# Kernel optimization log

Measured on AMD Instinct MI355X. Metric: run time of the kernel, lower is better.

## Reference

```python
import jax, jax.numpy as jnp
import numpy as np

N_NODES = 4096
D_MODEL = 1024
MAX_DEPS = 8
N_CLASSES = 64


def setup_inputs() -> dict:
    key = jax.random.key(0)
    k1, k2, k3 = jax.random.split(key, 3)
    questions = jax.random.normal(k1, (N_NODES, D_MODEL), dtype=jnp.float32)
    # Padded dependency lists; every dependency index is strictly < node index,
    # so processing nodes in index order is a valid topological order.
    rng = np.random.default_rng(0)
    dep_idx = np.zeros((N_NODES, MAX_DEPS), dtype=np.int32)
    dep_mask = np.zeros((N_NODES, MAX_DEPS), dtype=np.int32)
    for i in range(1, N_NODES):
        nd = int(rng.integers(1, MAX_DEPS + 1))
        dep_idx[i, :nd] = rng.integers(0, i, size=nd)
        dep_mask[i, :nd] = 1
    W1 = jax.random.normal(k2, (D_MODEL, 2 * D_MODEL), dtype=jnp.float32) * 0.02
    b1 = jnp.zeros((D_MODEL,), dtype=jnp.float32)
    W2 = jax.random.normal(k3, (N_CLASSES, D_MODEL), dtype=jnp.float32) * 0.02
    b2 = jnp.zeros((N_CLASSES,), dtype=jnp.float32)
    return {
        "questions": questions,
        "W1": W1,
        "b1": b1,
        "W2": W2,
        "b2": b2,
        "dep_idx": jnp.asarray(dep_idx),
        "dep_mask": jnp.asarray(dep_mask),
    }


def reference(questions, W1, b1, W2, b2, dep_idx, dep_mask):
    n_nodes, d_model = questions.shape

    def step(answers, xs):
        i, q, deps, mask = xs
        ctx = answers[deps]                       # [MAX_DEPS, d_model] gather
        m = mask.astype(q.dtype)
        # masked mean; all-zero mask -> zero context (matches torch zeros branch)
        ctx_mean = (ctx * m[:, None]).sum(0) / jnp.maximum(m.sum(), 1.0)
        combined = jnp.concatenate([q, ctx_mean])  # [2*d_model]
        h = jax.nn.gelu(combined @ W1.T + b1, approximate=False)
        return answers.at[i].set(h), None

    answers0 = jnp.zeros((n_nodes, d_model), dtype=questions.dtype)
    xs = (jnp.arange(n_nodes), questions, dep_idx, dep_mask)
    answers, _ = jax.lax.scan(step, answers0, xs)
    root_answer = answers[n_nodes - 1]            # root = last node in topo order
    return root_answer @ W2.T + b2                # [n_classes] logits
```

## Files before the change

### kernel.cpp

```cpp
#include <hip/hip_runtime.h>

#define NN 4096
#define DM 1024
#define MD 8
#define NW 256
#define NCOL 4
#define NT 512
#define NWAVE (NT / 64)
#define UR 4
#define MAXL 4097

#define MI_NLEV 0
#define MI_ROOTPOS 1
#define MI_ARRIVE 8
#define MI_LO 1024
#define MI_NL 6144
#define MI_PERM 10240
#define MI_DCNT 14336
#define MI_INV 18432
#define MI_DPOS 22528

typedef __attribute__((ext_vector_type(8))) short bf16x8;
typedef __attribute__((ext_vector_type(8))) unsigned short ushort8;
typedef __attribute__((ext_vector_type(4))) float f32x4;

__device__ __forceinline__ float gelu_f(float x) {
  return 0.5f * x * (1.0f + erff(x * 0.70710678118654752440f));
}
__device__ __forceinline__ unsigned short f2bf(float x) {
  unsigned int u = __builtin_bit_cast(unsigned int, x);
  u += 0x7FFFu + ((u >> 16) & 1u);
  return (unsigned short)(u >> 16);
}
__device__ __forceinline__ float bf2f(unsigned short v) {
  return __builtin_bit_cast(float, (unsigned int)v << 16);
}

__global__ __launch_bounds__(1024) void k_prologue(
    const int* __restrict__ dep_idx, const int* __restrict__ dep_mask,
    int* __restrict__ meta) {
  __shared__ int lvl[NN];
  __shared__ int cnt[2 * NN];
  __shared__ int pos[NN];
  __shared__ int liv[NN];
  __shared__ int s_changed, s_max;
  const int t = threadIdx.x;
  for (int i = t; i < NN; i += 1024) { lvl[i] = 0; pos[i] = 0; liv[i] = (i == NN - 1) ? 1 : 0; }
  for (int i = t; i < 2 * NN; i += 1024) cnt[i] = 0;
  if (t == 0) s_max = 0;
  __syncthreads();
  for (int u = 0; u < 4; ++u) {
    const int i = u * 1024 + t;
    const int4 d0 = *(const int4*)&dep_idx[i * MD];
    const int4 d1 = *(const int4*)&dep_idx[i * MD + 4];
    const int4 m0 = *(const int4*)&dep_mask[i * MD];
    const int4 m1 = *(const int4*)&dep_mask[i * MD + 4];
    int my = 0;
    for (;;) {
      if (t == 0) s_changed = 0;
      __syncthreads();
      int m = 0;
      if (m0.x) { int l = lvl[d0.x] + 1; m = m > l ? m : l; }
      if (m0.y) { int l = lvl[d0.y] + 1; m = m > l ? m : l; }
      if (m0.z) { int l = lvl[d0.z] + 1; m = m > l ? m : l; }
      if (m0.w) { int l = lvl[d0.w] + 1; m = m > l ? m : l; }
      if (m1.x) { int l = lvl[d1.x] + 1; m = m > l ? m : l; }
      if (m1.y) { int l = lvl[d1.y] + 1; m = m > l ? m : l; }
      if (m1.z) { int l = lvl[d1.z] + 1; m = m > l ? m : l; }
      if (m1.w) { int l = lvl[d1.w] + 1; m = m > l ? m : l; }
      if (m > my) { my = m; lvl[i] = m; s_changed = 1; }
      __syncthreads();
      if (!s_changed) break;
    }
  }
  for (int u = 3; u >= 0; --u) {
    const int i = u * 1024 + t;
    const int4 d0 = *(const int4*)&dep_idx[i * MD];
    const int4 d1 = *(const int4*)&dep_idx[i * MD + 4];
    const int4 m0 = *(const int4*)&dep_mask[i * MD];
    const int4 m1 = *(const int4*)&dep_mask[i * MD + 4];
    for (;;) {
      if (t == 0) s_changed = 0;
      __syncthreads();
      if (liv[i]) {
        if (m0.x && !liv[d0.x]) { liv[d0.x] = 1; s_changed = 1; }
        if (m0.y && !liv[d0.y]) { liv[d0.y] = 1; s_changed = 1; }
        if (m0.z && !liv[d0.z]) { liv[d0.z] = 1; s_changed = 1; }
        if (m0.w && !liv[d0.w]) { liv[d0.w] = 1; s_changed = 1; }
        if (m1.x && !liv[d1.x]) { liv[d1.x] = 1; s_changed = 1; }
        if (m1.y && !liv[d1.y]) { liv[d1.y] = 1; s_changed = 1; }
        if (m1.z && !liv[d1.z]) { liv[d1.z] = 1; s_changed = 1; }
        if (m1.w && !liv[d1.w]) { liv[d1.w] = 1; s_changed = 1; }
      }
      __syncthreads();
      if (!s_changed) break;
    }
  }
  for (int i = t; i < NN; i += 1024) {
    atomicAdd(&cnt[2 * lvl[i] + (liv[i] ? 0 : 1)], 1);
    atomicMax(&s_max, lvl[i]);
  }
  __syncthreads();
  const int nL = s_max + 1;
  if (t == 0) {
    int off = 0;
    for (int l = 0; l < nL; ++l) {
      meta[MI_LO + l] = off;
      meta[MI_NL + l] = cnt[2 * l];
      int a = cnt[2 * l], b = cnt[2 * l + 1];
      cnt[2 * l] = off; off += a;
      cnt[2 * l + 1] = off; off += b;
    }
    meta[MI_LO + nL] = off;
    meta[MI_NLEV] = nL;
  }
  __syncthreads();
  for (int i = t; i < NN; i += 1024)
    pos[i] = atomicAdd(&cnt[2 * lvl[i] + (liv[i] ? 0 : 1)], 1);
  __syncthreads();
  for (int i = t; i < NN; i += 1024) {
    const int r = pos[i];
    meta[MI_PERM + r] = i;
    int nd = 0;
    #pragma unroll
    for (int d = 0; d < MD; ++d) {
      if (dep_mask[i * MD + d]) { meta[MI_DPOS + r * MD + nd] = pos[dep_idx[i * MD + d]]; ++nd; }
    }
    for (int d = nd; d < MD; ++d) meta[MI_DPOS + r * MD + d] = 0;
    meta[MI_DCNT + r] = nd;
    ((float*)meta)[MI_INV + r] = nd ? 1.0f / (float)nd : 0.0f;
  }
  if (t == 0) meta[MI_ROOTPOS] = pos[NN - 1];
  for (int i = t; i < NW; i += 1024) meta[MI_ARRIVE + i] = 0;
}

__global__ __launch_bounds__(256) void k_cvtq(
    const float* __restrict__ Q, unsigned short* __restrict__ Qb) {
  const size_t i = ((size_t)blockIdx.x * 256 + threadIdx.x) * 8;
  float4 a = *(const float4*)&Q[i];
  float4 b = *(const float4*)&Q[i + 4];
  ushort8 o;
  o[0] = f2bf(a.x); o[1] = f2bf(a.y); o[2] = f2bf(a.z); o[3] = f2bf(a.w);
  o[4] = f2bf(b.x); o[5] = f2bf(b.y); o[6] = f2bf(b.z); o[7] = f2bf(b.w);
  *(ushort8*)&Qb[i] = o;
}

__global__ __launch_bounds__(256) void k_preq(
    const unsigned short* __restrict__ Qb, const float* __restrict__ W1,
    const float* __restrict__ b1, float* __restrict__ preQ) {
  const int t = threadIdx.x;
  const int wave = t >> 6, lane = t & 63;
  const int wm = wave >> 1, wn = wave & 1;
  const int m0 = blockIdx.y * 128 + wm * 64;
  const int n0 = blockIdx.x * 128 + wn * 64;
  const int lrow = lane & 15;
  const int klo = (lane >> 4) * 8;
  f32x4 acc[4][4] = {};
  for (int k0 = 0; k0 < DM; k0 += 32) {
    bf16x8 af[4];
    #pragma unroll
    for (int f = 0; f < 4; ++f)
      af[f] = *(const bf16x8*)&Qb[(size_t)(m0 + f * 16 + lrow) * DM + k0 + klo];
    bf16x8 bfr[4];
    #pragma unroll
    for (int g = 0; g < 4; ++g) {
      const float* wsrc = &W1[(size_t)(n0 + g * 16 + lrow) * 2048 + k0 + klo];
      float4 w0 = *(const float4*)&wsrc[0];
      float4 w1 = *(const float4*)&wsrc[4];
      bf16x8 bb;
      bb[0] = (short)f2bf(w0.x); bb[1] = (short)f2bf(w0.y);
      bb[2] = (short)f2bf(w0.z); bb[3] = (short)f2bf(w0.w);
      bb[4] = (short)f2bf(w1.x); bb[5] = (short)f2bf(w1.y);
      bb[6] = (short)f2bf(w1.z); bb[7] = (short)f2bf(w1.w);
      bfr[g] = bb;
    }
    #pragma unroll
    for (int f = 0; f < 4; ++f)
      #pragma unroll
      for (int g = 0; g < 4; ++g)
        acc[f][g] = __builtin_amdgcn_mfma_f32_16x16x32_bf16(af[f], bfr[g], acc[f][g], 0, 0, 0);
  }
  float b1v[4];
  #pragma unroll
  for (int g = 0; g < 4; ++g) b1v[g] = b1[n0 + g * 16 + lrow];
  const int mrow = (lane >> 4) * 4;
  #pragma unroll
  for (int f = 0; f < 4; ++f)
    #pragma unroll
    for (int g = 0; g < 4; ++g) {
      const int n = n0 + g * 16 + lrow;
      #pragma unroll
      for (int r = 0; r < 4; ++r)
        preQ[(size_t)(m0 + f * 16 + mrow + r) * DM + n] = acc[f][g][r] + b1v[g];
    }
}

__global__ __launch_bounds__(NT) void k_levels(
    const float* __restrict__ W1, const float* __restrict__ preQ,
    unsigned short* __restrict__ hPb, float4* __restrict__ gPan, int* __restrict__ meta) {
  const int tid = threadIdx.x;
  const int wb = blockIdx.x;
  const int c0 = wb * NCOL;
  const int wave = tid >> 6, lane = tid & 63;
  const int nL = meta[MI_NLEV];
  __shared__ int s_lo[MAXL];
  __shared__ int s_nl[MAXL];
  __shared__ float4 preLDS[NT];
  for (int i = tid; i <= nL; i += NT) s_lo[i] = meta[MI_LO + i];
  for (int i = tid; i < nL; i += NT) s_nl[i] = meta[MI_NL + i];
  __syncthreads();
  float4* gp = gPan + (size_t)wb * NN;
  const float* invA = (const float*)&meta[MI_INV];

  for (int l = 0; l < nL; ++l) {
    const int lo = s_lo[l];
    const int nA = s_nl[l];

    for (int r = lo + tid; r < lo + nA; r += NT) {
      const int node = meta[MI_PERM + r];
      const int nd = meta[MI_DCNT + r];
      const float iv = invA[r];
      const int4 p0 = *(const int4*)&meta[MI_DPOS + r * MD];
      const int4 p1 = *(const int4*)&meta[MI_DPOS + r * MD + 4];
      const int dps[8] = {p0.x, p0.y, p0.z, p0.w, p1.x, p1.y, p1.z, p1.w};
      float sx = 0.f, sy = 0.f, sz = 0.f, sw = 0.f;
      #pragma unroll
      for (int d = 0; d < MD; ++d) {
        float4 v = gp[dps[d]];
        sx += (d < nd) ? v.x : 0.f;
        sy += (d < nd) ? v.y : 0.f;
        sz += (d < nd) ? v.z : 0.f;
        sw += (d < nd) ? v.w : 0.f;
      }
      const float4 pq = (l > 0 && r == lo + tid) ? preLDS[tid]
                                                 : *(const float4*)&preQ[(size_t)node * DM + c0];
      const unsigned short h0 = f2bf(gelu_f(pq.x + sx * iv));
      const unsigned short h1 = f2bf(gelu_f(pq.y + sy * iv));
      const unsigned short h2 = f2bf(gelu_f(pq.z + sz * iv));
      const unsigned short h3 = f2bf(gelu_f(pq.w + sw * iv));
      const unsigned long long u = (unsigned long long)h0 | ((unsigned long long)h1 << 16)
                                 | ((unsigned long long)h2 << 32) | ((unsigned long long)h3 << 48);
      __hip_atomic_store((unsigned long long*)&hPb[(size_t)r * DM + c0], u,
                         __ATOMIC_RELAXED, __HIP_MEMORY_SCOPE_AGENT);
    }
    __syncthreads();
    if (tid == 0)
      __hip_atomic_store(&meta[MI_ARRIVE + wb], l + 1, __ATOMIC_RELAXED, __HIP_MEMORY_SCOPE_AGENT);
    if (l + 1 < nL && tid < s_nl[l + 1]) {
      const int node2 = meta[MI_PERM + s_lo[l + 1] + tid];
      preLDS[tid] = *(const float4*)&preQ[(size_t)node2 * DM + c0];
    }
    if (tid < 64) {
      for (;;) {
        int m = 1 << 30;
        #pragma unroll
        for (int u = 0; u < 4; ++u) {
          int v = __hip_atomic_load(&meta[MI_ARRIVE + tid * 4 + u], __ATOMIC_RELAXED, __HIP_MEMORY_SCOPE_AGENT);
          m = v < m ? v : m;
        }
        #pragma unroll
        for (int off = 1; off < 64; off <<= 1) {
          int o = __shfl_xor(m, off);
          m = o < m ? o : m;
        }
        if (m >= l + 1) break;
        __builtin_amdgcn_s_sleep(1);
      }
    }
    __syncthreads();

    for (int base = wave * UR; base < nA; base += NWAVE * UR) {
      const int cnt = nA - base;
      ushort8 hv[UR][2];
      #pragma unroll
      for (int u = 0; u < UR; ++u) {
        const int r = lo + base + ((u < cnt) ? u : 0);
        const ushort8* h8 = (const ushort8*)&hPb[(size_t)r * DM];
        hv[u][0] = h8[lane * 2];
        hv[u][1] = h8[lane * 2 + 1];
      }
      float rr[UR][NCOL];
      #pragma unroll
      for (int cc = 0; cc < NCOL; ++cc) {
        const float* wsrc = &W1[(size_t)(c0 + cc) * 2048 + 1024 + lane * 16];
        const float4 w0 = *(const float4*)&wsrc[0];
        const float4 w1 = *(const float4*)&wsrc[4];
        const float4 w2 = *(const float4*)&wsrc[8];
        const float4 w3 = *(const float4*)&wsrc[12];
        #pragma unroll
        for (int u = 0; u < UR; ++u) {
          float a = bf2f(hv[u][0][0]) * w0.x + bf2f(hv[u][0][1]) * w0.y
                  + bf2f(hv[u][0][2]) * w0.z + bf2f(hv[u][0][3]) * w0.w
                  + bf2f(hv[u][0][4]) * w1.x + bf2f(hv[u][0][5]) * w1.y
                  + bf2f(hv[u][0][6]) * w1.z + bf2f(hv[u][0][7]) * w1.w
                  + bf2f(hv[u][1][0]) * w2.x + bf2f(hv[u][1][1]) * w2.y
                  + bf2f(hv[u][1][2]) * w2.z + bf2f(hv[u][1][3]) * w2.w
                  + bf2f(hv[u][1][4]) * w3.x + bf2f(hv[u][1][5]) * w3.y
                  + bf2f(hv[u][1][6]) * w3.z + bf2f(hv[u][1][7]) * w3.w;
          rr[u][cc] = a;
        }
      }
      #pragma unroll
      for (int off = 1; off < 64; off <<= 1)
        #pragma unroll
        for (int u = 0; u < UR; ++u)
          #pragma unroll
          for (int cc = 0; cc < NCOL; ++cc)
            rr[u][cc] += __shfl_xor(rr[u][cc], off);
      if (lane == 0) {
        #pragma unroll
        for (int u = 0; u < UR; ++u)
          if (u < cnt) gp[lo + base + u] = make_float4(rr[u][0], rr[u][1], rr[u][2], rr[u][3]);
      }
    }
    __syncthreads();
  }
}

__global__ __launch_bounds__(256) void k_logits(
    const float* __restrict__ W2, const float* __restrict__ b2,
    const unsigned short* __restrict__ hPb, const int* __restrict__ meta,
    float* __restrict__ out) {
  __shared__ float red[256];
  const int t = threadIdx.x;
  const int row = meta[MI_ROOTPOS];
  const int j = t >> 2, kc = t & 3;
  const ushort8* h8 = (const ushort8*)&hPb[(size_t)row * DM];
  const float* wr = W2 + (size_t)j * DM;
  float acc = 0.f;
  for (int k = kc * 256; k < kc * 256 + 256; k += 8) {
    ushort8 hv = h8[k >> 3];
    float4 wa = *(const float4*)&wr[k];
    float4 wb = *(const float4*)&wr[k + 4];
    acc += bf2f(hv[0]) * wa.x + bf2f(hv[1]) * wa.y + bf2f(hv[2]) * wa.z + bf2f(hv[3]) * wa.w
         + bf2f(hv[4]) * wb.x + bf2f(hv[5]) * wb.y + bf2f(hv[6]) * wb.z + bf2f(hv[7]) * wb.w;
  }
  red[t] = acc;
  __syncthreads();
  if (kc == 0) out[j] = red[t] + red[t + 1] + red[t + 2] + red[t + 3] + b2[j];
}

extern "C" void kernel_launch(void* const* d_in, const int* in_sizes, int n_in,
                              void* d_out, int out_size, void* d_ws, size_t ws_size,
                              hipStream_t stream) {
  const float* Q        = (const float*)d_in[0];
  const float* W1       = (const float*)d_in[1];
  const float* b1       = (const float*)d_in[2];
  const float* W2       = (const float*)d_in[3];
  const float* b2       = (const float*)d_in[4];
  const int*   dep_idx  = (const int*)d_in[5];
  const int*   dep_mask = (const int*)d_in[6];

  char* ws = (char*)d_ws;
  float*          preQ = (float*)ws;
  unsigned short* hPb  = (unsigned short*)(ws + (16ull << 20));
  unsigned short* Qb   = (unsigned short*)(ws + (24ull << 20));
  float4*         gPan = (float4*)(ws + (32ull << 20));
  int*            meta = (int*)(ws + (48ull << 20));
  float*          out  = (float*)d_out;

  k_prologue<<<dim3(1), dim3(1024), 0, stream>>>(dep_idx, dep_mask, meta);
  k_cvtq<<<dim3((NN * DM) / (256 * 8)), dim3(256), 0, stream>>>(Q, Qb);
  k_preq<<<dim3(DM / 128, NN / 128), dim3(256), 0, stream>>>(Qb, W1, b1, preQ);
  k_levels<<<dim3(NW), dim3(NT), 0, stream>>>(W1, preQ, hPb, gPan, meta);
  k_logits<<<dim3(1), dim3(256), 0, stream>>>(W2, b2, hPb, meta, out);
}
```

Before: 557.1 us.

## Fuse bf16 conversion into prologue, wave-level graph analysis, fuse logits, hoist W1

Folds the Q-to-bf16 conversion into the prologue launch: block 0 does the graph analysis while the other 256 blocks do the conversion. The level and liveness fixed-point passes now run in a single wave. They use compact 16-bit dependency and level arrays in LDS and iterate with __any instead of block-wide barriers. The logits GEMV is folded into the tail of k_levels on block 0, and the per-block W1 context slice is hoisted into registers once instead of reloaded every level. The aim is to cut launch count and prologue barrier overhead. The trade-offs are large LDS per block in the conversion blocks, more register pressure in k_levels, and a dependence on the root row being fully written before block 0 reads it.

```diff
diff --git a/kernel.cpp b/kernel.cpp
--- a/kernel.cpp
+++ b/kernel.cpp
@@ -36,69 +36,92 @@
   return __builtin_bit_cast(float, (unsigned int)v << 16);
 }
 
-__global__ __launch_bounds__(1024) void k_prologue(
-    const int* __restrict__ dep_idx, const int* __restrict__ dep_mask,
-    int* __restrict__ meta) {
-  __shared__ int lvl[NN];
+__global__ __launch_bounds__(1024) void k_pro(
+    const float* __restrict__ Q, const int* __restrict__ dep_idx,
+    const int* __restrict__ dep_mask, int* __restrict__ meta,
+    unsigned short* __restrict__ Qb) {
+  __shared__ unsigned short deps[NN][MD];
+  __shared__ unsigned short lvl[NN];
+  __shared__ unsigned short liv[NN];
   __shared__ int cnt[2 * NN];
   __shared__ int pos[NN];
-  __shared__ int liv[NN];
-  __shared__ int s_changed, s_max;
+  __shared__ int s_max;
   const int t = threadIdx.x;
-  for (int i = t; i < NN; i += 1024) { lvl[i] = 0; pos[i] = 0; liv[i] = (i == NN - 1) ? 1 : 0; }
-  for (int i = t; i < 2 * NN; i += 1024) cnt[i] = 0;
-  if (t == 0) s_max = 0;
-  __syncthreads();
-  for (int u = 0; u < 4; ++u) {
-    const int i = u * 1024 + t;
+
+  if (blockIdx.x != 0) {
+    const size_t total = (size_t)NN * DM / 8;
+    for (size_t c = (size_t)(blockIdx.x - 1) * 1024 + t; c < total; c += 256 * 1024) {
+      const size_t i = c * 8;
+      float4 a = *(const float4*)&Q[i];
+      float4 b = *(const float4*)&Q[i + 4];
+      ushort8 o;
+      o[0] = f2bf(a.x); o[1] = f2bf(a.y); o[2] = f2bf(a.z); o[3] = f2bf(a.w);
+      o[4] = f2bf(b.x); o[5] = f2bf(b.y); o[6] = f2bf(b.z); o[7] = f2bf(b.w);
+      *(ushort8*)&Qb[i] = o;
+    }
+    return;
+  }
+
+  for (int i = t; i < NN; i += 1024) {
     const int4 d0 = *(const int4*)&dep_idx[i * MD];
     const int4 d1 = *(const int4*)&dep_idx[i * MD + 4];
     const int4 m0 = *(const int4*)&dep_mask[i * MD];
     const int4 m1 = *(const int4*)&dep_mask[i * MD + 4];
-    int my = 0;
-    for (;;) {
-      if (t == 0) s_changed = 0;
-      __syncthreads();
-      int m = 0;
-      if (m0.x) { int l = lvl[d0.x] + 1; m = m > l ? m : l; }
-      if (m0.y) { int l = lvl[d0.y] + 1; m = m > l ? m : l; }
-      if (m0.z) { int l = lvl[d0.z] + 1; m = m > l ? m : l; }
-      if (m0.w) { int l = lvl[d0.w] + 1; m = m > l ? m : l; }
-      if (m1.x) { int l = lvl[d1.x] + 1; m = m > l ? m : l; }
-      if (m1.y) { int l = lvl[d1.y] + 1; m = m > l ? m : l; }
-      if (m1.z) { int l = lvl[d1.z] + 1; m = m > l ? m : l; }
-      if (m1.w) { int l = lvl[d1.w] + 1; m = m > l ? m : l; }
-      if (m > my) { my = m; lvl[i] = m; s_changed = 1; }
-      __syncthreads();
-      if (!s_changed) break;
-    }
-  }
-  for (int u = 3; u >= 0; --u) {
-    const int i = u * 1024 + t;
-    const int4 d0 = *(const int4*)&dep_idx[i * MD];
-    const int4 d1 = *(const int4*)&dep_idx[i * MD + 4];
-    const int4 m0 = *(const int4*)&dep_mask[i * MD];
-    const int4 m1 = *(const int4*)&dep_mask[i * MD + 4];
-    for (;;) {
-      if (t == 0) s_changed = 0;
-      __syncthreads();
-      if (liv[i]) {
-        if (m0.x && !liv[d0.x]) { liv[d0.x] = 1; s_changed = 1; }
-        if (m0.y && !liv[d0.y]) { liv[d0.y] = 1; s_changed = 1; }
-        if (m0.z && !liv[d0.z]) { liv[d0.z] = 1; s_changed = 1; }
-        if (m0.w && !liv[d0.w]) { liv[d0.w] = 1; s_changed = 1; }
-        if (m1.x && !liv[d1.x]) { liv[d1.x] = 1; s_changed = 1; }
-        if (m1.y && !liv[d1.y]) { liv[d1.y] = 1; s_changed = 1; }
-        if (m1.z && !liv[d1.z]) { liv[d1.z] = 1; s_changed = 1; }
-        if (m1.w && !liv[d1.w]) { liv[d1.w] = 1; s_changed = 1; }
-      }
-      __syncthreads();
-      if (!s_changed) break;
-    }
-  }
+    deps[i][0] = m0.x ? (unsigned short)(d0.x + 1) : 0;
+    deps[i][1] = m0.y ? (unsigned short)(d0.y + 1) : 0;
+    deps[i][2] = m0.z ? (unsigned short)(d0.z + 1) : 0;
+    deps[i][3] = m0.w ? (unsigned short)(d0.w + 1) : 0;
+    deps[i][4] = m1.x ? (unsigned short)(d1.x + 1) : 0;
+    deps[i][5] = m1.y ? (unsigned short)(d1.y + 1) : 0;
+    deps[i][6] = m1.z ? (unsigned short)(d1.z + 1) : 0;
+    deps[i][7] = m1.w ? (unsigned short)(d1.w + 1) : 0;
+    lvl[i] = 0;
+    liv[i] = (i == NN - 1) ? 1 : 0;
+  }
+  for (int i = t; i < 2 * NN; i += 1024) cnt[i] = 0;
+  if (t == 0) s_max = 0;
+  __syncthreads();
+
+  if (t < 64) {
+    for (int grp = 0; grp < 64; ++grp) {
+      const int i = grp * 64 + t;
+      const ushort8 dr = *(const ushort8*)&deps[i][0];
+      int lvprev = -1;
+      for (;;) {
+        int m = 0;
+        #pragma unroll
+        for (int k = 0; k < MD; ++k) {
+          const int dd = dr[k];
+          if (dd) { const int l2 = (int)lvl[dd - 1] + 1; m = m > l2 ? m : l2; }
+        }
+        const bool ch = (m != lvprev);
+        lvprev = m;
+        lvl[i] = (unsigned short)m;
+        if (!__any(ch)) break;
+      }
+    }
+    for (int grp = 63; grp >= 0; --grp) {
+      const int i = grp * 64 + t;
+      const ushort8 dr = *(const ushort8*)&deps[i][0];
+      for (;;) {
+        bool ch = false;
+        if (liv[i]) {
+          #pragma unroll
+          for (int k = 0; k < MD; ++k) {
+            const int dd = dr[k];
+            if (dd && !liv[dd - 1]) { liv[dd - 1] = 1; ch = true; }
+          }
+        }
+        if (!__any(ch)) break;
+      }
+    }
+  }
+  __syncthreads();
+
   for (int i = t; i < NN; i += 1024) {
-    atomicAdd(&cnt[2 * lvl[i] + (liv[i] ? 0 : 1)], 1);
-    atomicMax(&s_max, lvl[i]);
+    const int lv = lvl[i];
+    atomicAdd(&cnt[2 * lv + (liv[i] ? 0 : 1)], 1);
+    atomicMax(&s_max, lv);
   }
   __syncthreads();
   const int nL = s_max + 1;
@@ -107,7 +130,7 @@
     for (int l = 0; l < nL; ++l) {
       meta[MI_LO + l] = off;
       meta[MI_NL + l] = cnt[2 * l];
-      int a = cnt[2 * l], b = cnt[2 * l + 1];
+      const int a = cnt[2 * l], b = cnt[2 * l + 1];
       cnt[2 * l] = off; off += a;
       cnt[2 * l + 1] = off; off += b;
     }
@@ -123,26 +146,16 @@
     meta[MI_PERM + r] = i;
     int nd = 0;
     #pragma unroll
-    for (int d = 0; d < MD; ++d) {
-      if (dep_mask[i * MD + d]) { meta[MI_DPOS + r * MD + nd] = pos[dep_idx[i * MD + d]]; ++nd; }
-    }
-    for (int d = nd; d < MD; ++d) meta[MI_DPOS + r * MD + d] = 0;
+    for (int k = 0; k < MD; ++k) {
+      const int dd = deps[i][k];
+      if (dd) { meta[MI_DPOS + r * MD + nd] = pos[dd - 1]; ++nd; }
+    }
+    for (int k = nd; k < MD; ++k) meta[MI_DPOS + r * MD + k] = 0;
     meta[MI_DCNT + r] = nd;
     ((float*)meta)[MI_INV + r] = nd ? 1.0f / (float)nd : 0.0f;
   }
   if (t == 0) meta[MI_ROOTPOS] = pos[NN - 1];
   for (int i = t; i < NW; i += 1024) meta[MI_ARRIVE + i] = 0;
-}
-
-__global__ __launch_bounds__(256) void k_cvtq(
-    const float* __restrict__ Q, unsigned short* __restrict__ Qb) {
-  const size_t i = ((size_t)blockIdx.x * 256 + threadIdx.x) * 8;
-  float4 a = *(const float4*)&Q[i];
-  float4 b = *(const float4*)&Q[i + 4];
-  ushort8 o;
-  o[0] = f2bf(a.x); o[1] = f2bf(a.y); o[2] = f2bf(a.z); o[3] = f2bf(a.w);
-  o[4] = f2bf(b.x); o[5] = f2bf(b.y); o[6] = f2bf(b.z); o[7] = f2bf(b.w);
-  *(ushort8*)&Qb[i] = o;
 }
 
 __global__ __launch_bounds__(256) void k_preq(
@@ -197,17 +210,25 @@
 
 __global__ __launch_bounds__(NT) void k_levels(
     const float* __restrict__ W1, const float* __restrict__ preQ,
-    unsigned short* __restrict__ hPb, float4* __restrict__ gPan, int* __restrict__ meta) {
+    unsigned short* __restrict__ hPb, float4* __restrict__ gPan, int* __restrict__ meta,
+    const float* __restrict__ W2, const float* __restrict__ b2, float* __restrict__ out) {
   const int tid = threadIdx.x;
   const int wb = blockIdx.x;
   const int c0 = wb * NCOL;
   const int wave = tid >> 6, lane = tid & 63;
   const int nL = meta[MI_NLEV];
+  const int rootRow = meta[MI_ROOTPOS];
   __shared__ int s_lo[MAXL];
   __shared__ int s_nl[MAXL];
   __shared__ float4 preLDS[NT];
   for (int i = tid; i <= nL; i += NT) s_lo[i] = meta[MI_LO + i];
   for (int i = tid; i < nL; i += NT) s_nl[i] = meta[MI_NL + i];
+  float4 wreg[NCOL][4];
+  #pragma unroll
+  for (int cc = 0; cc < NCOL; ++cc)
+    #pragma unroll
+    for (int q = 0; q < 4; ++q)
+      wreg[cc][q] = *(const float4*)&W1[(size_t)(c0 + cc) * 2048 + 1024 + lane * 16 + q * 4];
   __syncthreads();
   float4* gp = gPan + (size_t)wb * NN;
   const float* invA = (const float*)&meta[MI_INV];
@@ -281,22 +302,17 @@
       }
       float rr[UR][NCOL];
       #pragma unroll
-      for (int cc = 0; cc < NCOL; ++cc) {
-        const float* wsrc = &W1[(size_t)(c0 + cc) * 2048 + 1024 + lane * 16];
-        const float4 w0 = *(const float4*)&wsrc[0];
-        const float4 w1 = *(const float4*)&wsrc[4];
-        const float4 w2 = *(const float4*)&wsrc[8];
-        const float4 w3 = *(const float4*)&wsrc[12];
-        #pragma unroll
-        for (int u = 0; u < UR; ++u) {
-          float a = bf2f(hv[u][0][0]) * w0.x + bf2f(hv[u][0][1]) * w0.y
-                  + bf2f(hv[u][0][2]) * w0.z + bf2f(hv[u][0][3]) * w0.w
-                  + bf2f(hv[u][0][4]) * w1.x + bf2f(hv[u][0][5]) * w1.y
-                  + bf2f(hv[u][0][6]) * w1.z + bf2f(hv[u][0][7]) * w1.w
-                  + bf2f(hv[u][1][0]) * w2.x + bf2f(hv[u][1][1]) * w2.y
-                  + bf2f(hv[u][1][2]) * w2.z + bf2f(hv[u][1][3]) * w2.w
-                  + bf2f(hv[u][1][4]) * w3.x + bf2f(hv[u][1][5]) * w3.y
-                  + bf2f(hv[u][1][6]) * w3.z + bf2f(hv[u][1][7]) * w3.w;
+      for (int u = 0; u < UR; ++u) {
+        float hf[16];
+        #pragma unroll
+        for (int e = 0; e < 8; ++e) { hf[e] = bf2f(hv[u][0][e]); hf[8 + e] = bf2f(hv[u][1][e]); }
+        #pragma unroll
+        for (int cc = 0; cc < NCOL; ++cc) {
+          float a = 0.f;
+          #pragma unroll
+          for (int q = 0; q < 4; ++q)
+            a += hf[q * 4 + 0] * wreg[cc][q].x + hf[q * 4 + 1] * wreg[cc][q].y
+               + hf[q * 4 + 2] * wreg[cc][q].z + hf[q * 4 + 3] * wreg[cc][q].w;
           rr[u][cc] = a;
         }
       }
@@ -315,29 +331,29 @@
     }
     __syncthreads();
   }
-}
-
-__global__ __launch_bounds__(256) void k_logits(
-    const float* __restrict__ W2, const float* __restrict__ b2,
-    const unsigned short* __restrict__ hPb, const int* __restrict__ meta,
-    float* __restrict__ out) {
-  __shared__ float red[256];
-  const int t = threadIdx.x;
-  const int row = meta[MI_ROOTPOS];
-  const int j = t >> 2, kc = t & 3;
-  const ushort8* h8 = (const ushort8*)&hPb[(size_t)row * DM];
-  const float* wr = W2 + (size_t)j * DM;
-  float acc = 0.f;
-  for (int k = kc * 256; k < kc * 256 + 256; k += 8) {
-    ushort8 hv = h8[k >> 3];
-    float4 wa = *(const float4*)&wr[k];
-    float4 wb = *(const float4*)&wr[k + 4];
-    acc += bf2f(hv[0]) * wa.x + bf2f(hv[1]) * wa.y + bf2f(hv[2]) * wa.z + bf2f(hv[3]) * wa.w
-         + bf2f(hv[4]) * wb.x + bf2f(hv[5]) * wb.y + bf2f(hv[6]) * wb.z + bf2f(hv[7]) * wb.w;
-  }
-  red[t] = acc;
-  __syncthreads();
-  if (kc == 0) out[j] = red[t] + red[t + 1] + red[t + 2] + red[t + 3] + b2[j];
+
+  if (wb == 0) {
+    float* red = (float*)preLDS;
+    const int j = tid >> 3, kc = tid & 7;
+    const ushort8* h8 = (const ushort8*)&hPb[(size_t)rootRow * DM];
+    const float* wr2 = W2 + (size_t)j * DM;
+    float acc = 0.f;
+    for (int k = kc * 128; k < kc * 128 + 128; k += 8) {
+      ushort8 hv = h8[k >> 3];
+      float4 wa = *(const float4*)&wr2[k];
+      float4 wb4 = *(const float4*)&wr2[k + 4];
+      acc += bf2f(hv[0]) * wa.x + bf2f(hv[1]) * wa.y + bf2f(hv[2]) * wa.z + bf2f(hv[3]) * wa.w
+           + bf2f(hv[4]) * wb4.x + bf2f(hv[5]) * wb4.y + bf2f(hv[6]) * wb4.z + bf2f(hv[7]) * wb4.w;
+    }
+    red[tid] = acc;
+    __syncthreads();
+    if (kc == 0) {
+      float s = 0.f;
+      #pragma unroll
+      for (int e = 0; e < 8; ++e) s += red[j * 8 + e];
+      out[j] = s + b2[j];
+    }
+  }
 }
 
 extern "C" void kernel_launch(void* const* d_in, const int* in_sizes, int n_in,
@@ -359,9 +375,7 @@
   int*            meta = (int*)(ws + (48ull << 20));
   float*          out  = (float*)d_out;
 
-  k_prologue<<<dim3(1), dim3(1024), 0, stream>>>(dep_idx, dep_mask, meta);
-  k_cvtq<<<dim3((NN * DM) / (256 * 8)), dim3(256), 0, stream>>>(Q, Qb);
+  k_pro<<<dim3(257), dim3(1024), 0, stream>>>(Q, dep_idx, dep_mask, meta, Qb);
   k_preq<<<dim3(DM / 128, NN / 128), dim3(256), 0, stream>>>(Qb, W1, b1, preQ);
-  k_levels<<<dim3(NW), dim3(NT), 0, stream>>>(W1, preQ, hPb, gPan, meta);
-  k_logits<<<dim3(1), dim3(256), 0, stream>>>(W2, b2, hPb, meta, out);
-}
+  k_levels<<<dim3(NW), dim3(NT), 0, stream>>>(W1, preQ, hPb, gPan, meta, W2, b2, out);
+}
```

New measurement: 556.4 us. About the same (-0.1%).
